# Kernel tuning notes

Measured on AMD Instinct MI355X. Metric: run time of the kernel, lower is better.

## Reference

```python
import jax, jax.numpy as jnp
import numpy as np

N = 100000
E = 1600000
D_IN = 128
D_OUT = 128


def setup_inputs() -> dict:
    key = jax.random.key(0)
    k1, k2, k3, k4, k5 = jax.random.split(key, 5)
    X = jax.random.normal(k1, (N, D_IN), dtype=jnp.float32)
    # degrees holds d^{-1/2} style per-node normalization factors (positive)
    degrees = jax.random.uniform(k2, (N,), dtype=jnp.float32, minval=0.05, maxval=1.0)
    # CSR row pointers: sorted, anchored at 0 and E
    rp = jnp.sort(jax.random.randint(k3, (N + 1,), 0, E, dtype=jnp.int64))
    row_pointers = rp.at[0].set(0).at[-1].set(E)
    column_index = jax.random.randint(k4, (E,), 0, N, dtype=jnp.int64)
    # dense GCN weight, uniform(-stdv, stdv) with stdv = 1/sqrt(output_dim)
    stdv = 1.0 / np.sqrt(D_OUT)
    weights = jax.random.uniform(k5, (D_IN, D_OUT), dtype=jnp.float32, minval=-stdv, maxval=stdv)
    return {"X": X, "weights": weights, "degrees": degrees,
            "row_pointers": row_pointers, "column_index": column_index}


def _spmm_csr(row_pointers, column_index, degrees, H):
    """out[i] = sum_{e in row i} degrees[i]*degrees[col[e]] * H[col[e]] (symmetric GCN norm)."""
    n = row_pointers.shape[0] - 1
    e = column_index.shape[0]
    # map each edge to its destination row via the CSR pointer array
    row_id = jnp.searchsorted(row_pointers, jnp.arange(e), side="right") - 1  # [E]
    coef = degrees[row_id] * degrees[column_index]                             # [E]
    gathered = H[column_index] * coef[:, None]                                 # [E, D]
    return jax.ops.segment_sum(gathered, row_id, num_segments=n)               # [N, D]


def reference(X, weights, degrees, row_pointers, column_index):
    X_prime = X @ weights                      # dense projection [N, D_OUT]
    return _spmm_csr(row_pointers, column_index, degrees, X_prime)
```

## Files before the change

### kernel.cpp

```cpp
#include <hip/hip_runtime.h>
#include <hip/hip_bf16.h>

#define D 128

typedef __attribute__((ext_vector_type(8))) short bf16x8;
typedef __attribute__((ext_vector_type(4))) float f32x4;

static __device__ __forceinline__ ushort f2bf(float f) {
    __hip_bfloat16 h = __float2bfloat16(f);
    return *(ushort*)&h;
}
static __device__ __forceinline__ float bfl(uint u) { return __uint_as_float(u << 16); }
static __device__ __forceinline__ float bfh(uint u) { return __uint_as_float(u & 0xffff0000u); }

__global__ __launch_bounds__(256) void swizzle_w(const float* __restrict__ W,
                                                 ushort* __restrict__ Wz)
{
    const int t = blockIdx.x * 256 + threadIdx.x;
    const int lane = t & 63;
    const int combo = t >> 6;
    const int ks = combo >> 3, nb = combo & 7;
    const int krow = ks * 32 + ((lane >> 4) << 3);
    const int col  = nb * 16 + (lane & 15);
    ushort u[8];
    #pragma unroll
    for (int j = 0; j < 8; ++j) u[j] = f2bf(W[(krow + j) * D + col]);
    uint4 p;
    p.x = (uint)u[0] | ((uint)u[1] << 16);
    p.y = (uint)u[2] | ((uint)u[3] << 16);
    p.z = (uint)u[4] | ((uint)u[5] << 16);
    p.w = (uint)u[6] | ((uint)u[7] << 16);
    *(uint4*)(Wz + (size_t)t * 8) = p;
}

__global__ __launch_bounds__(256) void gemm_mfma(const float* __restrict__ X,
                                                 const ushort* __restrict__ Wz,
                                                 const float* __restrict__ deg,
                                                 ushort* __restrict__ Xp, int n)
{
    __shared__ ushort wsh[32 * 64 * 8];
    const int tid = threadIdx.x;
    {
        const uint4* src = (const uint4*)Wz;
        uint4* dst = (uint4*)wsh;
        #pragma unroll
        for (int i = 0; i < 8; ++i) dst[tid + i * 256] = src[tid + i * 256];
    }
    __syncthreads();

    const int lane = tid & 63;
    const int wave = tid >> 6;
    const int m = lane & 15, quad = lane >> 4;
    const int r0 = blockIdx.x * 128 + wave * 32;

    bf16x8 afrag[2][4];
    #pragma unroll
    for (int t = 0; t < 2; ++t) {
        long long arow = r0 + t * 16 + m;
        if (arow >= n) arow = n - 1;
        const float* xa = X + arow * D + quad * 8;
        #pragma unroll
        for (int ks = 0; ks < 4; ++ks) {
            float4 lo = *(const float4*)(xa + ks * 32);
            float4 hi = *(const float4*)(xa + ks * 32 + 4);
            bf16x8 a;
            a[0] = (short)f2bf(lo.x); a[1] = (short)f2bf(lo.y);
            a[2] = (short)f2bf(lo.z); a[3] = (short)f2bf(lo.w);
            a[4] = (short)f2bf(hi.x); a[5] = (short)f2bf(hi.y);
            a[6] = (short)f2bf(hi.z); a[7] = (short)f2bf(hi.w);
            afrag[t][ks] = a;
        }
    }

    f32x4 acc[2][8];
    #pragma unroll
    for (int t = 0; t < 2; ++t)
        #pragma unroll
        for (int nb = 0; nb < 8; ++nb) acc[t][nb] = (f32x4){0.f, 0.f, 0.f, 0.f};

    #pragma unroll
    for (int nb = 0; nb < 8; ++nb) {
        #pragma unroll
        for (int ks = 0; ks < 4; ++ks) {
            bf16x8 b = *(const bf16x8*)(wsh + ((size_t)((ks * 8 + nb) * 64 + lane)) * 8);
            acc[0][nb] = __builtin_amdgcn_mfma_f32_16x16x32_bf16(afrag[0][ks], b, acc[0][nb], 0, 0, 0);
            acc[1][nb] = __builtin_amdgcn_mfma_f32_16x16x32_bf16(afrag[1][ks], b, acc[1][nb], 0, 0, 0);
        }
    }

    #pragma unroll
    for (int t = 0; t < 2; ++t) {
        #pragma unroll
        for (int r = 0; r < 4; ++r) {
            const int row = r0 + t * 16 + quad * 4 + r;
            if (row < n) {
                const float dr = deg[row];
                #pragma unroll
                for (int nb = 0; nb < 8; ++nb)
                    Xp[(size_t)row * D + nb * 16 + m] = f2bf(dr * acc[t][nb][r]);
            }
        }
    }
}

__global__ __launch_bounds__(256) void spmm_csr(const ushort* __restrict__ Xp,
                                                const float* __restrict__ deg,
                                                const int* __restrict__ rp,
                                                const int* __restrict__ ci,
                                                float* __restrict__ out, int n)
{
    const int row = blockIdx.x * 16 + (threadIdx.x >> 4);
    if (row >= n) return;
    const int sub = threadIdx.x & 15;
    const int beg = rp[row], end = rp[row + 1];
    const uint4* Xq = (const uint4*)Xp;

    float a0 = 0.f, a1 = 0.f, a2 = 0.f, a3 = 0.f;
    float a4 = 0.f, a5 = 0.f, a6 = 0.f, a7 = 0.f;

#define ACCUM(v)                                          \
    do {                                                  \
        a0 += bfl((v).x); a1 += bfh((v).x);               \
        a2 += bfl((v).y); a3 += bfh((v).y);               \
        a4 += bfl((v).z); a5 += bfh((v).z);               \
        a6 += bfl((v).w); a7 += bfh((v).w);               \
    } while (0)

    int e = beg;
    for (; e + 4 <= end; e += 4) {
        int c0 = ci[e], c1 = ci[e + 1], c2 = ci[e + 2], c3 = ci[e + 3];
        uint4 v0 = Xq[(size_t)c0 * 16 + sub];
        uint4 v1 = Xq[(size_t)c1 * 16 + sub];
        uint4 v2 = Xq[(size_t)c2 * 16 + sub];
        uint4 v3 = Xq[(size_t)c3 * 16 + sub];
        ACCUM(v0); ACCUM(v1); ACCUM(v2); ACCUM(v3);
    }
    for (; e < end; ++e) {
        uint4 v = Xq[(size_t)ci[e] * 16 + sub];
        ACCUM(v);
    }
#undef ACCUM

    const float dr = deg[row];
    float4* op = (float4*)(out + (size_t)row * D + sub * 8);
    op[0] = make_float4(dr * a0, dr * a1, dr * a2, dr * a3);
    op[1] = make_float4(dr * a4, dr * a5, dr * a6, dr * a7);
}

extern "C" void kernel_launch(void* const* d_in, const int* in_sizes, int n_in,
                              void* d_out, int out_size, void* d_ws, size_t ws_size,
                              hipStream_t stream)
{
    const float* X   = (const float*)d_in[0];
    const float* W   = (const float*)d_in[1];
    const float* deg = (const float*)d_in[2];
    const int*   rp  = (const int*)d_in[3];
    const int*   ci  = (const int*)d_in[4];
    float* out = (float*)d_out;
    const int n = in_sizes[2];

    ushort* Xp = (ushort*)d_ws;
    ushort* Wz = Xp + (size_t)n * D;

    swizzle_w<<<8, 256, 0, stream>>>(W, Wz);
    gemm_mfma<<<(n + 127) / 128, 256, 0, stream>>>(X, Wz, deg, Xp, n);
    spmm_csr<<<(n + 15) / 16, 256, 0, stream>>>(Xp, deg, rp, ci, out, n);
}
```

Baseline: 183.9 us.

## Assign one wavefront per row in SpMM with scalar column indices

The SpMM kernel moves from 16 threads per row to a full 64-lane wavefront per row. Each lane now loads one 32-bit word (two bf16 values) per neighbor, and the row index is made wave-uniform with readfirstlane so the CSR indices can be loaded through the scalar path. The main loop is unrolled 8 edges deep with two accumulator pairs to keep more gathers in flight, and the remainder is handled by a clamped, predicated batch of 8. The aim is to increase memory-level parallelism and lower index-load overhead, at the cost of 4x more blocks and smaller per-lane loads.

Result: faster. 176.9 us (-3.8%).

```diff
diff --git a/kernel.cpp b/kernel.cpp
--- a/kernel.cpp
+++ b/kernel.cpp
@@ -109,42 +109,61 @@
                                                 const int* __restrict__ ci,
                                                 float* __restrict__ out, int n)
 {
-    const int row = blockIdx.x * 16 + (threadIdx.x >> 4);
-    if (row >= n) return;
-    const int sub = threadIdx.x & 15;
-    const int beg = rp[row], end = rp[row + 1];
-    const uint4* Xq = (const uint4*)Xp;
+    int row = __builtin_amdgcn_readfirstlane(blockIdx.x * 4 + (threadIdx.x >> 6));
+    if (row >= n) row = n - 1;
+    const int lane = threadIdx.x & 63;
+    const int beg = rp[row];
+    const int end = rp[row + 1];
+    const uint* __restrict__ Xq = (const uint*)Xp;
 
-    float a0 = 0.f, a1 = 0.f, a2 = 0.f, a3 = 0.f;
-    float a4 = 0.f, a5 = 0.f, a6 = 0.f, a7 = 0.f;
-
-#define ACCUM(v)                                          \
-    do {                                                  \
-        a0 += bfl((v).x); a1 += bfh((v).x);               \
-        a2 += bfl((v).y); a3 += bfh((v).y);               \
-        a4 += bfl((v).z); a5 += bfh((v).z);               \
-        a6 += bfl((v).w); a7 += bfh((v).w);               \
-    } while (0)
+    float a0 = 0.f, a1 = 0.f;
+    float b0 = 0.f, b1 = 0.f;
 
     int e = beg;
-    for (; e + 4 <= end; e += 4) {
-        int c0 = ci[e], c1 = ci[e + 1], c2 = ci[e + 2], c3 = ci[e + 3];
-        uint4 v0 = Xq[(size_t)c0 * 16 + sub];
-        uint4 v1 = Xq[(size_t)c1 * 16 + sub];
-        uint4 v2 = Xq[(size_t)c2 * 16 + sub];
-        uint4 v3 = Xq[(size_t)c3 * 16 + sub];
-        ACCUM(v0); ACCUM(v1); ACCUM(v2); ACCUM(v3);
+    for (; e + 8 <= end; e += 8) {
+        const int c0 = ci[e + 0], c1 = ci[e + 1], c2 = ci[e + 2], c3 = ci[e + 3];
+        const int c4 = ci[e + 4], c5 = ci[e + 5], c6 = ci[e + 6], c7 = ci[e + 7];
+        const uint v0 = Xq[(size_t)c0 * 64 + lane];
+        const uint v1 = Xq[(size_t)c1 * 64 + lane];
+        const uint v2 = Xq[(size_t)c2 * 64 + lane];
+        const uint v3 = Xq[(size_t)c3 * 64 + lane];
+        const uint v4 = Xq[(size_t)c4 * 64 + lane];
+        const uint v5 = Xq[(size_t)c5 * 64 + lane];
+        const uint v6 = Xq[(size_t)c6 * 64 + lane];
+        const uint v7 = Xq[(size_t)c7 * 64 + lane];
+        a0 += bfl(v0); a1 += bfh(v0);
+        b0 += bfl(v1); b1 += bfh(v1);
+        a0 += bfl(v2); a1 += bfh(v2);
+        b0 += bfl(v3); b1 += bfh(v3);
+        a0 += bfl(v4); a1 += bfh(v4);
+        b0 += bfl(v5); b1 += bfh(v5);
+        a0 += bfl(v6); a1 += bfh(v6);
+        b0 += bfl(v7); b1 += bfh(v7);
     }
-    for (; e < end; ++e) {
-        uint4 v = Xq[(size_t)ci[e] * 16 + sub];
-        ACCUM(v);
+
+    if (e < end) {
+        int cc[8];
+        #pragma unroll
+        for (int j = 0; j < 8; ++j) {
+            const int ee = e + j;
+            cc[j] = ci[ee < end ? ee : end - 1];
+        }
+        uint vv[8];
+        #pragma unroll
+        for (int j = 0; j < 8; ++j) vv[j] = Xq[(size_t)cc[j] * 64 + lane];
+        #pragma unroll
+        for (int j = 0; j < 8; ++j) {
+            if (e + j < end) {
+                a0 += bfl(vv[j]); a1 += bfh(vv[j]);
+            }
+        }
     }
-#undef ACCUM
 
     const float dr = deg[row];
-    float4* op = (float4*)(out + (size_t)row * D + sub * 8);
-    op[0] = make_float4(dr * a0, dr * a1, dr * a2, dr * a3);
-    op[1] = make_float4(dr * a4, dr * a5, dr * a6, dr * a7);
+    float2 o;
+    o.x = dr * (a0 + b0);
+    o.y = dr * (a1 + b1);
+    *(float2*)(out + (size_t)row * D + lane * 2) = o;
 }
 
 extern "C" void kernel_launch(void* const* d_in, const int* in_sizes, int n_in,
@@ -164,5 +183,5 @@
 
     swizzle_w<<<8, 256, 0, stream>>>(W, Wz);
     gemm_mfma<<<(n + 127) / 128, 256, 0, stream>>>(X, Wz, deg, Xp, n);
-    spmm_csr<<<(n + 15) / 16, 256, 0, stream>>>(Xp, deg, rp, ci, out, n);
+    spmm_csr<<<(n + 3) / 4, 256, 0, stream>>>(Xp, deg, rp, ci, out, n);
 }
```

## Restructure SpMM to wave-per-8-rows edge streaming with double-buffered gathers

Applied to the files above, without the earlier changes.

The SpMM kernel now gives each 64-lane wave a contiguous run of 8 rows and streams their edges in batches of 8. Each lane loads one 4-byte bf16 pair instead of 16 lanes loading 16-byte chunks. Two batches of gathers are kept in flight (double buffering) and row boundaries are detected inside the edge stream, so short or empty rows no longer leave lanes idle. The cost is more per-edge branching, narrower per-lane loads, and serial row-boundary handling within a wave.

Measured after the change: 187.5 us. No clear change (+1.9%).

```diff
diff --git a/kernel.cpp b/kernel.cpp
--- a/kernel.cpp
+++ b/kernel.cpp
@@ -103,48 +103,93 @@
     }
 }
 
+#define ROWS_PER_WAVE 8
+
+#define ISSUE(V, ebase, cnt)                                              \
+    do {                                                                  \
+        int _rem = eend - (ebase);                                        \
+        (cnt) = _rem > 8 ? 8 : _rem;                                      \
+        int _c[8];                                                        \
+        if ((cnt) == 8) {               \
+            _Pragma("unroll")                                             \
+            for (int _j = 0; _j < 8; ++_j) _c[_j] = ci[(ebase) + _j];     \
+        } else {                           \
+            _Pragma("unroll")                                             \
+            for (int _j = 0; _j < 8; ++_j)                                \
+                _c[_j] = ci[(ebase) + (_j < (cnt) ? _j : 0)];             \
+        }                                                                 \
+        _Pragma("unroll")                                                 \
+        for (int _j = 0; _j < 8; ++_j)                                    \
+            V[_j] = Xq[(size_t)_c[_j] * 64 + lane];                       \
+    } while (0)
+
+#define ACCUM(V, ebase, cnt)                                              \
+    do {                                                                  \
+        _Pragma("unroll")                                                 \
+        for (int _j = 0; _j < 8; ++_j) {                                  \
+            if (_j < (cnt)) {                                             \
+                while ((ebase) + _j >= bnd) {      \
+                    const float _dr = deg[row];                           \
+                    float2 _o;                                            \
+                    _o.x = _dr * (a0 + b0);                               \
+                    _o.y = _dr * (a1 + b1);                               \
+                    *(float2*)(out + (size_t)row * D + lane * 2) = _o;    \
+                    a0 = a1 = b0 = b1 = 0.f;                              \
+                    ++row;                                                \
+                    bnd = rp[row + 1];                                    \
+                }                                                         \
+                if (_j & 1) { b0 += bfl(V[_j]); b1 += bfh(V[_j]); }       \
+                else        { a0 += bfl(V[_j]); a1 += bfh(V[_j]); }       \
+            }                                                             \
+        }                                                                 \
+    } while (0)
+
 __global__ __launch_bounds__(256) void spmm_csr(const ushort* __restrict__ Xp,
                                                 const float* __restrict__ deg,
                                                 const int* __restrict__ rp,
                                                 const int* __restrict__ ci,
                                                 float* __restrict__ out, int n)
 {
-    const int row = blockIdx.x * 16 + (threadIdx.x >> 4);
-    if (row >= n) return;
-    const int sub = threadIdx.x & 15;
-    const int beg = rp[row], end = rp[row + 1];
-    const uint4* Xq = (const uint4*)Xp;
-
-    float a0 = 0.f, a1 = 0.f, a2 = 0.f, a3 = 0.f;
-    float a4 = 0.f, a5 = 0.f, a6 = 0.f, a7 = 0.f;
-
-#define ACCUM(v)                                          \
-    do {                                                  \
-        a0 += bfl((v).x); a1 += bfh((v).x);               \
-        a2 += bfl((v).y); a3 += bfh((v).y);               \
-        a4 += bfl((v).z); a5 += bfh((v).z);               \
-        a6 += bfl((v).w); a7 += bfh((v).w);               \
-    } while (0)
-
-    int e = beg;
-    for (; e + 4 <= end; e += 4) {
-        int c0 = ci[e], c1 = ci[e + 1], c2 = ci[e + 2], c3 = ci[e + 3];
-        uint4 v0 = Xq[(size_t)c0 * 16 + sub];
-        uint4 v1 = Xq[(size_t)c1 * 16 + sub];
-        uint4 v2 = Xq[(size_t)c2 * 16 + sub];
-        uint4 v3 = Xq[(size_t)c3 * 16 + sub];
-        ACCUM(v0); ACCUM(v1); ACCUM(v2); ACCUM(v3);
-    }
-    for (; e < end; ++e) {
-        uint4 v = Xq[(size_t)ci[e] * 16 + sub];
-        ACCUM(v);
-    }
-#undef ACCUM
-
-    const float dr = deg[row];
-    float4* op = (float4*)(out + (size_t)row * D + sub * 8);
-    op[0] = make_float4(dr * a0, dr * a1, dr * a2, dr * a3);
-    op[1] = make_float4(dr * a4, dr * a5, dr * a6, dr * a7);
+    const int r0 = __builtin_amdgcn_readfirstlane(
+        (blockIdx.x * 4 + (threadIdx.x >> 6)) * ROWS_PER_WAVE);
+    if (r0 >= n) return;
+    const int rend = (r0 + ROWS_PER_WAVE < n) ? r0 + ROWS_PER_WAVE : n;
+    const int lane = threadIdx.x & 63;
+    const uint* __restrict__ Xq = (const uint*)Xp;
+
+    int e    = rp[r0];
+    const int eend = rp[rend];
+    int row  = r0;
+    int bnd  = rp[row + 1];
+
+    float a0 = 0.f, a1 = 0.f, b0 = 0.f, b1 = 0.f;
+
+    uint vA[8], vB[8];
+    int eA = e, cntA = 0;
+    if (eA < eend) { ISSUE(vA, eA, cntA); e = eA + cntA; }
+    int eB = e, cntB = 0;
+    if (eB < eend) { ISSUE(vB, eB, cntB); e = eB + cntB; }
+
+    for (;;) {
+        if (cntA == 0) break;
+        ACCUM(vA, eA, cntA);
+        eA = e; cntA = 0;
+        if (eA < eend) { ISSUE(vA, eA, cntA); e = eA + cntA; }
+        if (cntB == 0) break;
+        ACCUM(vB, eB, cntB);
+        eB = e; cntB = 0;
+        if (eB < eend) { ISSUE(vB, eB, cntB); e = eB + cntB; }
+    }
+
+    while (row < rend) {
+        const float dr = deg[row];
+        float2 o;
+        o.x = dr * (a0 + b0);
+        o.y = dr * (a1 + b1);
+        *(float2*)(out + (size_t)row * D + lane * 2) = o;
+        a0 = a1 = b0 = b1 = 0.f;
+        ++row;
+    }
 }
 
 extern "C" void kernel_launch(void* const* d_in, const int* in_sizes, int n_in,
@@ -162,7 +207,10 @@
     ushort* Xp = (ushort*)d_ws;
     ushort* Wz = Xp + (size_t)n * D;
 
+    const int waves  = (n + ROWS_PER_WAVE - 1) / ROWS_PER_WAVE;
+    const int blocks = (waves + 3) / 4;
+
     swizzle_w<<<8, 256, 0, stream>>>(W, Wz);
     gemm_mfma<<<(n + 127) / 128, 256, 0, stream>>>(X, Wz, deg, Xp, n);
-    spmm_csr<<<(n + 15) / 16, 256, 0, stream>>>(Xp, deg, rp, ci, out, n);
-}
+    spmm_csr<<<blocks, 256, 0, stream>>>(Xp, deg, rp, ci, out, n);
+}
```
